# Optimization experiments

Measured on AMD Instinct MI355X. Metric: run time of the kernel, lower is better.

The kernel has to match this reference:

```python
import jax, jax.numpy as jnp
import numpy as np

N_NODES = 2048
N_EDGES = 8192
EDGE_DIM = 10
EDGE_HIDDEN = 32
HID = 160


def nnconv(x, edge_index, edge_attr, w1, b1, w2, b2, root, bias):
    """PyG-style NNConv with aggr='mean'.
    x: [N, HID], edge_attr: [E, EDGE_DIM], edge_index: [2, E] (src, dst).
    Per-edge weight W_e = MLP(e) reshaped to [HID, HID]; message = x[src] @ W_e,
    mean-aggregated at dst, plus root transform and bias.
    """
    n = x.shape[0]
    h = jax.nn.relu(edge_attr @ w1 + b1)                     # [E, EDGE_HIDDEN]
    W = (h @ w2 + b2).reshape(-1, HID, HID)                  # [E, HID, HID]
    src, dst = edge_index[0], edge_index[1]
    msg = jnp.einsum('ei,eio->eo', x[src], W)                # [E, HID]
    summed = jax.ops.segment_sum(msg, dst, num_segments=n)   # [N, HID]
    cnt = jax.ops.segment_sum(jnp.ones((msg.shape[0],), x.dtype), dst,
                              num_segments=n)
    aggr = summed / jnp.maximum(cnt, 1.0)[:, None]           # mean; 0 for isolated
    return aggr + x @ root + bias


def setup_inputs() -> dict:
    key = jax.random.key(0)
    ks = jax.random.split(key, 16)
    s = 1.0 / np.sqrt(HID)
    se = 1.0 / np.sqrt(EDGE_DIM)
    sh = 1.0 / np.sqrt(EDGE_HIDDEN)
    inp = {
        'x': jax.random.normal(ks[0], (N_NODES, HID), jnp.float32),
        'edge_attr': jax.random.uniform(ks[1], (N_EDGES, EDGE_DIM), jnp.float32),
        # conv1 (subgraph_conv1) params
        'w1_a': jax.random.normal(ks[2], (EDGE_DIM, EDGE_HIDDEN), jnp.float32) * se,
        'b1_a': jnp.zeros((EDGE_HIDDEN,), jnp.float32),
        'w2_a': jax.random.normal(ks[3], (EDGE_HIDDEN, HID * HID), jnp.float32) * sh,
        'b2_a': jnp.zeros((HID * HID,), jnp.float32),
        'root_a': jax.random.normal(ks[4], (HID, HID), jnp.float32) * s,
        'bias_a': jnp.zeros((HID,), jnp.float32),
        # conv2 (subgraph_conv2, applied twice) params
        'w1_b': jax.random.normal(ks[5], (EDGE_DIM, EDGE_HIDDEN), jnp.float32) * se,
        'b1_b': jnp.zeros((EDGE_HIDDEN,), jnp.float32),
        'w2_b': jax.random.normal(ks[6], (EDGE_HIDDEN, HID * HID), jnp.float32) * sh,
        'b2_b': jnp.zeros((HID * HID,), jnp.float32),
        'root_b': jax.random.normal(ks[7], (HID, HID), jnp.float32) * s,
        'bias_b': jnp.zeros((HID,), jnp.float32),
        'edge_index': jax.random.randint(ks[8], (2, N_EDGES), 0, N_NODES, jnp.int64),
    }
    return inp


def reference(x, edge_attr, w1_a, b1_a, w2_a, b2_a, root_a, bias_a,
              w1_b, b1_b, w2_b, b2_b, root_b, bias_b, edge_index):
    # subgraph_conv1 -> ReLU -> subgraph_conv2 -> ReLU -> subgraph_conv2
    h = jax.nn.relu(nnconv(x, edge_index, edge_attr,
                           w1_a, b1_a, w2_a, b2_a, root_a, bias_a))
    h = jax.nn.relu(nnconv(h, edge_index, edge_attr,
                           w1_b, b1_b, w2_b, b2_b, root_b, bias_b))
    h = nnconv(h, edge_index, edge_attr,
               w1_b, b1_b, w2_b, b2_b, root_b, bias_b)
    return h
```

## Files before the change

### kernel.cpp

```cpp
#include <hip/hip_runtime.h>

#define NN 2048
#define NE 8192
#define ED 10
#define EH 32
#define HID 160
#define KT 5440
#define KS 10
#define KSL 544
#define MT 32
#define APAD 552
#define NNH (NN * HID)

typedef __attribute__((ext_vector_type(8))) short short8;
typedef __attribute__((ext_vector_type(4))) float f32x4;
typedef unsigned int u32;

__device__ __forceinline__ ushort f2bf(float v) {
    u32 u = __float_as_uint(v);
    u += 0x7FFF + ((u >> 16) & 1);
    return (ushort)(u >> 16);
}
__device__ __forceinline__ u32 packbf(float lo, float hi) {
    return ((u32)f2bf(hi) << 16) | f2bf(lo);
}
__device__ __forceinline__ void gl2lds16(const ushort* g, ushort* l) {
    __builtin_amdgcn_global_load_lds(
        (const __attribute__((address_space(1))) u32*)g,
        (__attribute__((address_space(3))) u32*)l, 16, 0, 0);
}

__global__ __launch_bounds__(1024) void k_prep(
        const float* __restrict__ ea,
        const float* __restrict__ w1a, const float* __restrict__ b1a,
        const float* __restrict__ w1b, const float* __restrict__ b1b,
        float* __restrict__ ha, float* __restrict__ hb,
        const float* __restrict__ w2a, const float* __restrict__ b2a,
        const float* __restrict__ roota,
        const float* __restrict__ w2b, const float* __restrict__ b2b,
        const float* __restrict__ rootb,
        ushort* __restrict__ WcA, ushort* __restrict__ WcB,
        const int* __restrict__ ei, int* __restrict__ doff,
        int* __restrict__ degg, float* __restrict__ dinv,
        int2* __restrict__ delist2) {
    __shared__ __align__(16) char smem[21760];
    int b = blockIdx.x, t = threadIdx.x;

    if (b < 128) {
        int set = b >> 6, rel = b & 63;
        const float* w1 = set ? w1b : w1a;
        const float* b1 = set ? b1b : b1a;
        float* h = set ? hb : ha;
        int idx = rel * 4096 + t * 4;
        int e = idx >> 5, j0 = idx & 31;
        float o4[4];
#pragma unroll
        for (int u = 0; u < 4; ++u) {
            float acc = b1[j0 + u];
#pragma unroll
            for (int i = 0; i < ED; ++i) acc += ea[e * ED + i] * w1[i * EH + j0 + u];
            o4[u] = fmaxf(acc, 0.f);
        }
        *(float4*)&h[idx] = *(const float4*)o4;
        return;
    }
    if (b < 288) {
        int rel = b - 128;
        int set = rel / 80, i0 = (rel % 80) * 2;
        u32 (*tile)[34] = (u32(*)[34])smem;
        const float* w2 = set ? w2b : w2a;
        const float* b2 = set ? b2b : b2a;
        const float* root = set ? rootb : roota;
        ushort* W = set ? WcB : WcA;
        if (t < HID) {
#pragma unroll
            for (int di = 0; di < 2; ++di) {
                int i = i0 + di;
#pragma unroll
                for (int p = 0; p < 16; ++p) {
                    float v0 = w2[(size_t)(2 * p) * 25600 + i * HID + t];
                    float v1 = w2[(size_t)(2 * p + 1) * 25600 + i * HID + t];
                    tile[t][di * 17 + p] = packbf(v0, v1);
                }
                tile[t][di * 17 + 16] = packbf(b2[i * HID + t], root[i * HID + t]);
            }
        }
        __syncthreads();
        u32* dst = (u32*)W;
        for (int w = t; w < 5440; w += 1024) {
            int o = w / 34, j = w - o * 34;
            dst[(size_t)o * 2720 + i0 * 17 + j] = tile[o][j];
        }
        return;
    }
    int* deg = (int*)smem;
    int* cur = deg + NN;
    int* part = cur + NN;
    for (int i = t; i < NN; i += 1024) deg[i] = 0;
    __syncthreads();
    for (int e = t; e < NE; e += 1024) atomicAdd(&deg[ei[NE + e]], 1);
    __syncthreads();
    int loc[2], s = 0;
#pragma unroll
    for (int i = 0; i < 2; ++i) { loc[i] = s; s += deg[t * 2 + i]; }
    part[t] = s;
    __syncthreads();
    int tot = s;
    for (int st = 1; st < 1024; st <<= 1) {
        int v = (t >= st) ? part[t - st] : 0;
        __syncthreads();
        part[t] += v;
        __syncthreads();
    }
    int base = part[t] - tot;
#pragma unroll
    for (int i = 0; i < 2; ++i) {
        int d = t * 2 + i;
        doff[d] = base + loc[i];
        cur[d] = base + loc[i];
        degg[d] = deg[d];
        dinv[d] = 1.0f / fmaxf((float)deg[d], 1.0f);
    }
    __syncthreads();
    for (int e = t; e < NE; e += 1024) {
        int d = ei[NE + e];
        int src = ei[e];
        int p = atomicAdd(&cur[d], 1);
        delist2[p] = make_int2(e, src);
    }
}

__global__ __launch_bounds__(256) void k_layer(
        const float* __restrict__ xin,
        const float* __restrict__ h, const ushort* __restrict__ wc,
        const int2* __restrict__ delist2, const int* __restrict__ doff,
        const int* __restrict__ degg, const float* __restrict__ dinv,
        float* __restrict__ Cp) {
    __shared__ __align__(16) ushort sA[MT * APAD];
    __shared__ __align__(16) ushort sB[2][160 * 32];
    int t = threadIdx.x;
    int bm = blockIdx.x, ks = blockIdx.y;
    int d0 = bm * MT, i0 = ks * 16;

    auto stage = [&](int buf, int c) {
        size_t k0 = (size_t)ks * KSL + c * 32;
#pragma unroll
        for (int q = 0; q < 2; ++q) {
            int s = t + q * 256;
            int row = s >> 2;
            int lkq = (s & 3) ^ ((row >> 1) & 3);
            gl2lds16(&wc[(size_t)row * KT + k0 + lkq * 8], &sB[buf][s * 8]);
        }
        if (t < 128) {
            int s = t + 512;
            int row = s >> 2;
            int lkq = (s & 3) ^ ((row >> 1) & 3);
            gl2lds16(&wc[(size_t)row * KT + k0 + lkq * 8], &sB[buf][s * 8]);
        }
    };
    stage(0, 0);

    int il = t & 15, i = i0 + il;
    int dA = d0 + (t >> 4), dB = dA + 16;
    float accA[33], accB[33];
#pragma unroll
    for (int q = 0; q < 33; ++q) { accA[q] = 0.f; accB[q] = 0.f; }

    int aLo = doff[dA], aHi = aLo + degg[dA];
    for (int o = aLo; o < aHi; ++o) {
        int2 es = delist2[o];
        float xs = xin[es.y * HID + i];
        const float4* hp = (const float4*)&h[(size_t)es.x * EH];
#pragma unroll
        for (int q8 = 0; q8 < 8; ++q8) {
            float4 hv = hp[q8];
            accA[q8 * 4 + 0] += hv.x * xs;
            accA[q8 * 4 + 1] += hv.y * xs;
            accA[q8 * 4 + 2] += hv.z * xs;
            accA[q8 * 4 + 3] += hv.w * xs;
        }
        accA[32] += xs;
    }
    int bLo = doff[dB], bHi = bLo + degg[dB];
    for (int o = bLo; o < bHi; ++o) {
        int2 es = delist2[o];
        float xs = xin[es.y * HID + i];
        const float4* hp = (const float4*)&h[(size_t)es.x * EH];
#pragma unroll
        for (int q8 = 0; q8 < 8; ++q8) {
            float4 hv = hp[q8];
            accB[q8 * 4 + 0] += hv.x * xs;
            accB[q8 * 4 + 1] += hv.y * xs;
            accB[q8 * 4 + 2] += hv.z * xs;
            accB[q8 * 4 + 3] += hv.w * xs;
        }
        accB[32] += xs;
    }
    float rootA = xin[dA * HID + i], rootB = xin[dB * HID + i];

    {
        float diA = dinv[dA], diB = dinv[dB];
        u32* pa = (u32*)&sA[(t >> 4) * APAD + il * 34];
        u32* pb = (u32*)&sA[((t >> 4) + 16) * APAD + il * 34];
#pragma unroll
        for (int p = 0; p < 16; ++p) {
            pa[p] = packbf(accA[2 * p] * diA, accA[2 * p + 1] * diA);
            pb[p] = packbf(accB[2 * p] * diB, accB[2 * p + 1] * diB);
        }
        pa[16] = packbf(accA[32] * diA, rootA);
        pb[16] = packbf(accB[32] * diB, rootB);
    }
    __syncthreads();

    int wid = t >> 6, lane = t & 63;
    int wm = (wid >> 1) * 16, wn = (wid & 1) * 80;
    int lr = lane & 15, lk = lane >> 4;
    f32x4 acc[5];
#pragma unroll
    for (int j = 0; j < 5; ++j) acc[j] = (f32x4){0.f, 0.f, 0.f, 0.f};

    for (int c = 0; c < 17; ++c) {
        int cur = c & 1;
        if (c + 1 < 17) stage(cur ^ 1, c + 1);
        short8 av = *(const short8*)&sA[(wm + lr) * APAD + c * 32 + lk * 8];
        short8 bv[5];
#pragma unroll
        for (int nt = 0; nt < 5; ++nt) {
            int row = wn + nt * 16 + lr;
            bv[nt] = *(const short8*)&sB[cur][row * 32 +
                                             (lk ^ ((row >> 1) & 3)) * 8];
        }
#pragma unroll
        for (int nt = 0; nt < 5; ++nt)
            acc[nt] = __builtin_amdgcn_mfma_f32_16x16x32_bf16(av, bv[nt], acc[nt], 0, 0, 0);
        __syncthreads();
    }

    float* Cb = Cp + (size_t)ks * NNH;
#pragma unroll
    for (int nt = 0; nt < 5; ++nt) {
        int n = wn + nt * 16 + lr;
        int m0 = d0 + wm + lk * 4;
#pragma unroll
        for (int r = 0; r < 4; ++r)
            Cb[(size_t)(m0 + r) * HID + n] = acc[nt][r];
    }
}

__global__ __launch_bounds__(256) void k_fin(const float* __restrict__ Cp,
                                             const float* __restrict__ bias,
                                             float* __restrict__ xout, int dorelu) {
    int base = (blockIdx.x * 256 + threadIdx.x) * 4;
    float4 s = *(const float4*)&bias[base % HID];
#pragma unroll
    for (int p = 0; p < KS; ++p) {
        float4 v = *(const float4*)&Cp[(size_t)p * NNH + base];
        s.x += v.x; s.y += v.y; s.z += v.z; s.w += v.w;
    }
    if (dorelu) {
        s.x = fmaxf(s.x, 0.f); s.y = fmaxf(s.y, 0.f);
        s.z = fmaxf(s.z, 0.f); s.w = fmaxf(s.w, 0.f);
    }
    *(float4*)&xout[base] = s;
}

extern "C" void kernel_launch(void* const* d_in, const int* in_sizes, int n_in,
                              void* d_out, int out_size, void* d_ws, size_t ws_size,
                              hipStream_t stream) {
    const float* x     = (const float*)d_in[0];
    const float* ea    = (const float*)d_in[1];
    const float* w1a   = (const float*)d_in[2];
    const float* b1a   = (const float*)d_in[3];
    const float* w2a   = (const float*)d_in[4];
    const float* b2a   = (const float*)d_in[5];
    const float* roota = (const float*)d_in[6];
    const float* biasa = (const float*)d_in[7];
    const float* w1b   = (const float*)d_in[8];
    const float* b1b   = (const float*)d_in[9];
    const float* w2b   = (const float*)d_in[10];
    const float* b2b   = (const float*)d_in[11];
    const float* rootb = (const float*)d_in[12];
    const float* biasb = (const float*)d_in[13];
    const int*   ei    = (const int*)d_in[14];
    float* out = (float*)d_out;

    char* p = (char*)d_ws;
    float* Cp    = (float*)p;  p += (size_t)KS * NNH * 4;
    float* xacc0 = (float*)p;  p += (size_t)NNH * 4;
    float* xacc1 = (float*)p;  p += (size_t)NNH * 4;
    ushort* WcA  = (ushort*)p; p += (size_t)HID * KT * 2;
    ushort* WcB  = (ushort*)p; p += (size_t)HID * KT * 2;
    float* h_a   = (float*)p;  p += (size_t)NE * EH * 4;
    float* h_b   = (float*)p;  p += (size_t)NE * EH * 4;
    int* doff    = (int*)p;    p += NN * 4;
    int* degg    = (int*)p;    p += NN * 4;
    float* dinv  = (float*)p;  p += NN * 4;
    int2* delist2 = (int2*)p;  p += NE * 8;

    k_prep<<<289, 1024, 0, stream>>>(ea, w1a, b1a, w1b, b1b, h_a, h_b,
                                     w2a, b2a, roota, w2b, b2b, rootb, WcA, WcB,
                                     ei, doff, degg, dinv, delist2);

    dim3 lg(NN / MT, KS);
    k_layer<<<lg, 256, 0, stream>>>(x, h_a, WcA, delist2, doff, degg, dinv, Cp);
    k_fin<<<NNH / 1024, 256, 0, stream>>>(Cp, biasa, xacc0, 1);
    k_layer<<<lg, 256, 0, stream>>>(xacc0, h_b, WcB, delist2, doff, degg, dinv, Cp);
    k_fin<<<NNH / 1024, 256, 0, stream>>>(Cp, biasb, xacc1, 1);
    k_layer<<<lg, 256, 0, stream>>>(xacc1, h_b, WcB, delist2, doff, degg, dinv, Cp);
    k_fin<<<NNH / 1024, 256, 0, stream>>>(Cp, biasb, out, 0);
}
```

Before: 213.3 us.

## Load B fragments directly to registers, store bf16 partials, widen prep blocks

The layer kernel no longer stages the weight matrix through LDS with async global-to-LDS copies and per-chunk barriers. Each wave now loads its B fragments straight from global memory into double-buffered registers, with a launch-bounds occupancy hint of 2. Split-K partial results are stored as bf16 instead of fp32, halving the partial-buffer traffic, at the cost of extra rounding error before the final sum. The prep kernel now packs 4 rows per block instead of 2, which cuts the block count.

```diff
diff --git a/kernel.cpp b/kernel.cpp
--- a/kernel.cpp
+++ b/kernel.cpp
@@ -21,13 +21,11 @@
     u += 0x7FFF + ((u >> 16) & 1);
     return (ushort)(u >> 16);
 }
+__device__ __forceinline__ float bf2f(ushort u) {
+    return __uint_as_float(((u32)u) << 16);
+}
 __device__ __forceinline__ u32 packbf(float lo, float hi) {
     return ((u32)f2bf(hi) << 16) | f2bf(lo);
-}
-__device__ __forceinline__ void gl2lds16(const ushort* g, ushort* l) {
-    __builtin_amdgcn_global_load_lds(
-        (const __attribute__((address_space(1))) u32*)g,
-        (__attribute__((address_space(3))) u32*)l, 16, 0, 0);
 }
 
 __global__ __launch_bounds__(1024) void k_prep(
@@ -43,7 +41,7 @@
         const int* __restrict__ ei, int* __restrict__ doff,
         int* __restrict__ degg, float* __restrict__ dinv,
         int2* __restrict__ delist2) {
-    __shared__ __align__(16) char smem[21760];
+    __shared__ __align__(16) char smem[43520];
     int b = blockIdx.x, t = threadIdx.x;
 
     if (b < 128) {
@@ -64,32 +62,30 @@
         *(float4*)&h[idx] = *(const float4*)o4;
         return;
     }
-    if (b < 288) {
+    if (b < 208) {
         int rel = b - 128;
-        int set = rel / 80, i0 = (rel % 80) * 2;
-        u32 (*tile)[34] = (u32(*)[34])smem;
+        int set = rel / 40, i0 = (rel % 40) * 4;
+        u32 (*tile)[160][17] = (u32(*)[160][17])smem;
         const float* w2 = set ? w2b : w2a;
         const float* b2 = set ? b2b : b2a;
         const float* root = set ? rootb : roota;
         ushort* W = set ? WcB : WcA;
-        if (t < HID) {
-#pragma unroll
-            for (int di = 0; di < 2; ++di) {
-                int i = i0 + di;
-#pragma unroll
-                for (int p = 0; p < 16; ++p) {
-                    float v0 = w2[(size_t)(2 * p) * 25600 + i * HID + t];
-                    float v1 = w2[(size_t)(2 * p + 1) * 25600 + i * HID + t];
-                    tile[t][di * 17 + p] = packbf(v0, v1);
-                }
-                tile[t][di * 17 + 16] = packbf(b2[i * HID + t], root[i * HID + t]);
+        int di = t >> 8, o = t & 255;
+        if (o < HID) {
+            int i = i0 + di;
+#pragma unroll
+            for (int p = 0; p < 16; ++p) {
+                float v0 = w2[(size_t)(2 * p) * 25600 + i * HID + o];
+                float v1 = w2[(size_t)(2 * p + 1) * 25600 + i * HID + o];
+                tile[di][o][p] = packbf(v0, v1);
             }
+            tile[di][o][16] = packbf(b2[i * HID + o], root[i * HID + o]);
         }
         __syncthreads();
         u32* dst = (u32*)W;
-        for (int w = t; w < 5440; w += 1024) {
-            int o = w / 34, j = w - o * 34;
-            dst[(size_t)o * 2720 + i0 * 17 + j] = tile[o][j];
+        for (int w = t; w < 4 * HID * 17; w += 1024) {
+            int o2 = w / 68, rem = w - o2 * 68;
+            dst[(size_t)o2 * 2720 + i0 * 17 + rem] = tile[rem / 17][o2][rem % 17];
         }
         return;
     }
@@ -130,35 +126,16 @@
     }
 }
 
-__global__ __launch_bounds__(256) void k_layer(
+__global__ __launch_bounds__(256, 2) void k_layer(
         const float* __restrict__ xin,
         const float* __restrict__ h, const ushort* __restrict__ wc,
         const int2* __restrict__ delist2, const int* __restrict__ doff,
         const int* __restrict__ degg, const float* __restrict__ dinv,
-        float* __restrict__ Cp) {
+        ushort* __restrict__ Cp) {
     __shared__ __align__(16) ushort sA[MT * APAD];
-    __shared__ __align__(16) ushort sB[2][160 * 32];
     int t = threadIdx.x;
     int bm = blockIdx.x, ks = blockIdx.y;
     int d0 = bm * MT, i0 = ks * 16;
-
-    auto stage = [&](int buf, int c) {
-        size_t k0 = (size_t)ks * KSL + c * 32;
-#pragma unroll
-        for (int q = 0; q < 2; ++q) {
-            int s = t + q * 256;
-            int row = s >> 2;
-            int lkq = (s & 3) ^ ((row >> 1) & 3);
-            gl2lds16(&wc[(size_t)row * KT + k0 + lkq * 8], &sB[buf][s * 8]);
-        }
-        if (t < 128) {
-            int s = t + 512;
-            int row = s >> 2;
-            int lkq = (s & 3) ^ ((row >> 1) & 3);
-            gl2lds16(&wc[(size_t)row * KT + k0 + lkq * 8], &sB[buf][s * 8]);
-        }
-    };
-    stage(0, 0);
 
     int il = t & 15, i = i0 + il;
     int dA = d0 + (t >> 4), dB = dA + 16;
@@ -210,52 +187,59 @@
         pa[16] = packbf(accA[32] * diA, rootA);
         pb[16] = packbf(accB[32] * diB, rootB);
     }
-    __syncthreads();
 
     int wid = t >> 6, lane = t & 63;
     int wm = (wid >> 1) * 16, wn = (wid & 1) * 80;
     int lr = lane & 15, lk = lane >> 4;
+    const ushort* bp[5];
+#pragma unroll
+    for (int nt = 0; nt < 5; ++nt)
+        bp[nt] = wc + (size_t)(wn + nt * 16 + lr) * KT + ks * KSL + lk * 8;
+
     f32x4 acc[5];
 #pragma unroll
     for (int j = 0; j < 5; ++j) acc[j] = (f32x4){0.f, 0.f, 0.f, 0.f};
-
+    short8 bA[5], bB[5];
+#pragma unroll
+    for (int nt = 0; nt < 5; ++nt) bA[nt] = *(const short8*)&bp[nt][0];
+
+    __syncthreads();
+
+#pragma unroll
     for (int c = 0; c < 17; ++c) {
-        int cur = c & 1;
-        if (c + 1 < 17) stage(cur ^ 1, c + 1);
+        short8* bc = (c & 1) ? bB : bA;
+        short8* bn = (c & 1) ? bA : bB;
+        if (c + 1 < 17) {
+#pragma unroll
+            for (int nt = 0; nt < 5; ++nt)
+                bn[nt] = *(const short8*)&bp[nt][(c + 1) * 32];
+        }
         short8 av = *(const short8*)&sA[(wm + lr) * APAD + c * 32 + lk * 8];
-        short8 bv[5];
-#pragma unroll
-        for (int nt = 0; nt < 5; ++nt) {
-            int row = wn + nt * 16 + lr;
-            bv[nt] = *(const short8*)&sB[cur][row * 32 +
-                                             (lk ^ ((row >> 1) & 3)) * 8];
-        }
 #pragma unroll
         for (int nt = 0; nt < 5; ++nt)
-            acc[nt] = __builtin_amdgcn_mfma_f32_16x16x32_bf16(av, bv[nt], acc[nt], 0, 0, 0);
-        __syncthreads();
-    }
-
-    float* Cb = Cp + (size_t)ks * NNH;
+            acc[nt] = __builtin_amdgcn_mfma_f32_16x16x32_bf16(av, bc[nt], acc[nt], 0, 0, 0);
+    }
+
+    ushort* Cb = Cp + (size_t)ks * NNH;
 #pragma unroll
     for (int nt = 0; nt < 5; ++nt) {
         int n = wn + nt * 16 + lr;
         int m0 = d0 + wm + lk * 4;
 #pragma unroll
         for (int r = 0; r < 4; ++r)
-            Cb[(size_t)(m0 + r) * HID + n] = acc[nt][r];
-    }
-}
-
-__global__ __launch_bounds__(256) void k_fin(const float* __restrict__ Cp,
+            Cb[(size_t)(m0 + r) * HID + n] = f2bf(acc[nt][r]);
+    }
+}
+
+__global__ __launch_bounds__(256) void k_fin(const ushort* __restrict__ Cp,
                                              const float* __restrict__ bias,
                                              float* __restrict__ xout, int dorelu) {
     int base = (blockIdx.x * 256 + threadIdx.x) * 4;
     float4 s = *(const float4*)&bias[base % HID];
 #pragma unroll
     for (int p = 0; p < KS; ++p) {
-        float4 v = *(const float4*)&Cp[(size_t)p * NNH + base];
-        s.x += v.x; s.y += v.y; s.z += v.z; s.w += v.w;
+        ushort4 v = *(const ushort4*)&Cp[(size_t)p * NNH + base];
+        s.x += bf2f(v.x); s.y += bf2f(v.y); s.z += bf2f(v.z); s.w += bf2f(v.w);
     }
     if (dorelu) {
         s.x = fmaxf(s.x, 0.f); s.y = fmaxf(s.y, 0.f);
@@ -285,7 +269,7 @@
     float* out = (float*)d_out;
 
     char* p = (char*)d_ws;
-    float* Cp    = (float*)p;  p += (size_t)KS * NNH * 4;
+    ushort* Cp   = (ushort*)p; p += (size_t)KS * NNH * 2;
     float* xacc0 = (float*)p;  p += (size_t)NNH * 4;
     float* xacc1 = (float*)p;  p += (size_t)NNH * 4;
     ushort* WcA  = (ushort*)p; p += (size_t)HID * KT * 2;
@@ -297,7 +281,7 @@
     float* dinv  = (float*)p;  p += NN * 4;
     int2* delist2 = (int2*)p;  p += NE * 8;
 
-    k_prep<<<289, 1024, 0, stream>>>(ea, w1a, b1a, w1b, b1b, h_a, h_b,
+    k_prep<<<209, 1024, 0, stream>>>(ea, w1a, b1a, w1b, b1b, h_a, h_b,
                                      w2a, b2a, roota, w2b, b2b, rootb, WcA, WcB,
                                      ei, doff, degg, dinv, delist2);
 
```

After: 241.7 us. 13.3% more time.
